# Performance work log

Measured on AMD Instinct MI355X. Metric: run time of the kernel, lower is better.

The kernel has to match this reference:

```python
import jax, jax.numpy as jnp
import numpy as np
from jax import lax


def setup_inputs() -> dict:
    key = jax.random.key(0)
    k1, k2, k3, k4 = jax.random.split(key, 4)
    H = 2048
    L = 3
    hidden_states = jax.random.normal(k1, (2, 4096, H), dtype=jnp.float32)
    Win = jax.random.normal(k2, (3 * H, H), dtype=jnp.float32) * (H ** -0.5)
    conv_w = jax.random.normal(k3, (H, 1, L), dtype=jnp.float32) * (L ** -0.5)
    Wout = jax.random.normal(k4, (H, H), dtype=jnp.float32) * (H ** -0.5)
    return {"hidden_states": hidden_states, "Win": Win, "conv_w": conv_w, "Wout": Wout}


def reference(hidden_states, Win, conv_w, Wout):
    H = hidden_states.shape[-1]
    L = conv_w.shape[-1]
    BCx = jnp.einsum('bsh,oh->bso', hidden_states, Win)  # (b, s, 3H)
    B, C, x = jnp.split(BCx, 3, axis=-1)
    Bx = jnp.transpose(B * x, (0, 2, 1))  # (b, H, s)
    # depthwise causal conv: left-pad L-1 so output length == s (torch pads both
    # sides then slices [..., :seqlen]; left-only padding is equivalent)
    conv_out = lax.conv_general_dilated(
        Bx, conv_w, window_strides=(1,), padding=[(L - 1, 0)],
        feature_group_count=H, dimension_numbers=('NCH', 'OIH', 'NCH'))
    y = C * jnp.transpose(conv_out, (0, 2, 1))  # (b, s, H)
    return jnp.einsum('bsh,oh->bso', y, Wout)
```

## Files before the change

kernel.cpp:

```cpp
#include <hip/hip_runtime.h>
#include <hip/hip_bf16.h>

typedef unsigned short u16;
typedef __attribute__((ext_vector_type(8))) short bf16x8;
typedef __attribute__((ext_vector_type(4))) float f32x4;

static __device__ __forceinline__ u16 f2bf(float f) {
    unsigned u = __float_as_uint(f);
    unsigned r = (u + 0x7fffu + ((u >> 16) & 1u)) >> 16;
    return (u16)r;
}
static __device__ __forceinline__ float bf2f(u16 u) {
    return __uint_as_float(((unsigned)u) << 16);
}

static __device__ __forceinline__ void async_copy16(const void* gptr, void* lptr) {
    __builtin_amdgcn_global_load_lds(
        (const __attribute__((address_space(1))) void*)gptr,
        (__attribute__((address_space(3))) void*)lptr, 16, 0, 0);
}

__global__ __launch_bounds__(256)
void cvt_all(const float* __restrict__ a, const float* __restrict__ b,
             const float* __restrict__ c,
             u16* __restrict__ oa, u16* __restrict__ ob, u16* __restrict__ oc) {
#pragma unroll
    for (int it = 0; it < 8; it++) {
        long li = ((long)it << 20) + (long)blockIdx.x * 256 + threadIdx.x;
        const float* src; u16* dst; long u;
        if (li < 4194304)      { src = a; dst = oa; u = li; }
        else if (li < 7340032) { src = b; dst = ob; u = li - 4194304; }
        else                   { src = c; dst = oc; u = li - 7340032; }
        long i = u * 4;
        float4 f = *(const float4*)(src + i);
        u16 o[4] = { f2bf(f.x), f2bf(f.y), f2bf(f.z), f2bf(f.w) };
        *(uint2*)(dst + i) = *(const uint2*)o;
    }
}

template<bool BF16_OUT>
__global__ __launch_bounds__(512, 2)
void gemm_bt8(const u16* __restrict__ A, const u16* __restrict__ B,
              void* __restrict__ Cout, int M, int N, int K) {
    __shared__ __align__(16) u16 lds[65536];

    const int t    = threadIdx.x;
    const int lane = t & 63;
    const int wm   = (t >> 6) >> 2;
    const int wn   = (t >> 6) & 3;
    const int l15  = lane & 15;
    const int hi   = lane >> 4;
    const int l7   = lane & 7;

    const int nCols = N >> 8;
    const int TPB   = nCols >> 3;
    const int xcd   = blockIdx.x & 7;
    const int slot  = blockIdx.x >> 3;
    const long rowA = (long)slot * 256;
    long rowB = (long)xcd * TPB * 256;

    const int pl0 = t >> 3;
    const int slotcol = ((t & 7) ^ (pl0 & 7)) * 8;
    const u16* Asrc[2][2];
    const u16* Bsrc[2][2];
#pragma unroll
    for (int h = 0; h < 2; h++) {
        Asrc[h][0] = A + (rowA + h * 64 + pl0) * (long)K + slotcol;
        Asrc[h][1] = A + (rowA + 128 + h * 64 + pl0) * (long)K + slotcol;
    }
    auto SET_B = [&](long rB) {
#pragma unroll
        for (int h = 0; h < 2; h++) {
            int nb = (pl0 >> 5) * 64 + h * 32 + (pl0 & 31);
            Bsrc[h][0] = B + (rB + nb) * (long)K + slotcol;
            Bsrc[h][1] = Bsrc[h][0] + 128 * (long)K;
        }
    };
    SET_B(rowB);
    const int t8 = t * 8;

    auto STAGE_A = [&](int bufo, int h, int kk) {
        u16* d = lds + bufo + h * 8192 + t8;
        async_copy16(Asrc[h][0] + kk, d);
        async_copy16(Asrc[h][1] + kk, d + 4096);
    };
    auto STAGE_B = [&](int bufo, int h, int kk) {
        u16* d = lds + bufo + 16384 + h * 8192 + t8;
        async_copy16(Bsrc[h][0] + kk, d);
        async_copy16(Bsrc[h][1] + kk, d + 4096);
    };

    const int aBase = wm * 4096 + l15 * 64;
    const int bBase = 16384 + wn * 2048 + l15 * 64;
    const int sOff0 = (hi ^ l7) * 8;
    const int sOff1 = ((4 + hi) ^ l7) * 8;

    bf16x8 af[4][2], ba[2][2], bb[2][2];
    f32x4 acc[8][4] = {};

    auto LOAD_A2 = [&](int bufo, int Mq, int mb) {
        const u16* p = lds + bufo + Mq * 8192 + aBase + mb * 1024;
        af[mb][0]     = *(const bf16x8*)(p + sOff0);
        af[mb][1]     = *(const bf16x8*)(p + sOff1);
        af[mb + 1][0] = *(const bf16x8*)(p + 1024 + sOff0);
        af[mb + 1][1] = *(const bf16x8*)(p + 1024 + sOff1);
    };
    auto LOAD_B = [&](bf16x8 (&bg)[2][2], int bufo, int Nq) {
        const u16* p = lds + bufo + Nq * 8192 + bBase;
        bg[0][0] = *(const bf16x8*)(p + sOff0);
        bg[0][1] = *(const bf16x8*)(p + sOff1);
        bg[1][0] = *(const bf16x8*)(p + 1024 + sOff0);
        bg[1][1] = *(const bf16x8*)(p + 1024 + sOff1);
    };
    auto MFMA_H = [&](int Mq, int Nq, int mb, bf16x8 (&bg)[2][2]) {
        __builtin_amdgcn_s_setprio(1);
#pragma unroll
        for (int ks = 0; ks < 2; ks++)
#pragma unroll
            for (int m = mb; m < mb + 2; m++)
#pragma unroll
                for (int n = 0; n < 2; n++)
                    acc[Mq * 4 + m][Nq * 2 + n] =
                        __builtin_amdgcn_mfma_f32_16x16x32_bf16(
                            af[m][ks], bg[n][ks], acc[Mq * 4 + m][Nq * 2 + n],
                            0, 0, 0);
        __builtin_amdgcn_s_setprio(0);
    };

#define BAR()   __builtin_amdgcn_s_barrier()
#define SB()    __builtin_amdgcn_sched_barrier(0)
#define LGKM(n) do { asm volatile("s_waitcnt lgkmcnt(" #n ")" ::: "memory"); \
                     __builtin_amdgcn_sched_barrier(0); } while (0)
#define VM(n)   asm volatile("s_waitcnt vmcnt(" #n ")" ::: "memory")

#define TILE(BC, BN, KK)                                                     \
                                                              \
    LOAD_B(ba, BC, 0); LOAD_A2(BC, 0, 0); SB(); LOAD_A2(BC, 0, 2);           \
    STAGE_A(BN, 0, KK); STAGE_B(BN, 0, KK);                                  \
    LGKM(4); MFMA_H(0, 0, 0, ba); LGKM(0); MFMA_H(0, 0, 2, ba); BAR();       \
                                                              \
    LOAD_B(bb, BC, 1);                                                       \
    STAGE_B(BN, 1, KK); STAGE_A(BN, 1, KK);                                  \
    LGKM(0); MFMA_H(0, 1, 0, bb); MFMA_H(0, 1, 2, bb); BAR();                \
                                                              \
    LOAD_A2(BC, 1, 0); SB(); LOAD_A2(BC, 1, 2);                              \
    LGKM(4); MFMA_H(1, 1, 0, bb); LGKM(0); MFMA_H(1, 1, 2, bb); BAR();       \
                                                              \
    VM(0);                                                                   \
    MFMA_H(1, 0, 0, ba); MFMA_H(1, 0, 2, ba); BAR();

    STAGE_A(0, 0, 0);  STAGE_B(0, 0, 0);
    STAGE_A(0, 1, 0);  STAGE_B(0, 1, 0);
    asm volatile("s_waitcnt vmcnt(0)" ::: "memory");
    BAR();

    const int NT = K >> 6;
#pragma unroll 1
    for (int j = 0; j < TPB; j++) {
        const long rowBc = rowB;
#pragma unroll 1
        for (int i = 0; i < NT - 2; i += 2) {
            TILE(0, 32768, (i + 1) << 6);
            TILE(32768, 0, (i + 2) << 6);
        }
        TILE(0, 32768, (NT - 1) << 6);
        if (j + 1 < TPB) { rowB += 256; SET_B(rowB); }
        TILE(32768, 0, 0);

        const long crowBase = rowA + wm * 128 + hi * 4;
        const long ccolBase = rowBc + wn * 64 + l15;
#pragma unroll
        for (int mi = 0; mi < 8; mi++) {
#pragma unroll
            for (int nj = 0; nj < 4; nj++) {
                long base = (crowBase + mi * 16) * N + ccolBase + nj * 16;
#pragma unroll
                for (int r = 0; r < 4; r++) {
                    float v = acc[mi][nj][r];
                    long idx = base + (long)r * N;
                    if (BF16_OUT) ((u16*)Cout)[idx] = f2bf(v);
                    else          ((float*)Cout)[idx] = v;
                }
            }
        }
        if (j + 1 < TPB) {
#pragma unroll
            for (int mi = 0; mi < 8; mi++)
#pragma unroll
                for (int nj = 0; nj < 4; nj++)
#pragma unroll
                    for (int r = 0; r < 4; r++)
                        acc[mi][nj][r] = 0.0f;
        }
    }
    asm volatile("s_waitcnt vmcnt(0) lgkmcnt(0)" ::: "memory");

#undef TILE
#undef VM
#undef LGKM
#undef SB
#undef BAR
}

union U16x8 { uint4 v; u16 u[8]; };

__global__ __launch_bounds__(256)
void conv_fuse(const u16* __restrict__ BCx, const float* __restrict__ cw,
               u16* __restrict__ y) {
    const int r0 = blockIdx.x * 4;
    const int h0 = threadIdx.x * 8;
    const int batch = r0 >> 12;

    U16x8 Bv[6], Xv[6], Cv[4];
#pragma unroll
    for (int ii = 0; ii < 6; ii++) {
        int g = r0 - 2 + ii;
        if (g >= 0 && (g >> 12) == batch) {
            const u16* rp = BCx + (long)g * 6144;
            Bv[ii].v = *(const uint4*)(rp + h0);
            Xv[ii].v = *(const uint4*)(rp + 4096 + h0);
        } else {
            Bv[ii].v = make_uint4(0, 0, 0, 0);
            Xv[ii].v = make_uint4(0, 0, 0, 0);
        }
    }
#pragma unroll
    for (int jj = 0; jj < 4; jj++)
        Cv[jj].v = *(const uint4*)(BCx + (long)(r0 + jj) * 6144 + 2048 + h0);

    float bx[6][8];
#pragma unroll
    for (int ii = 0; ii < 6; ii++)
#pragma unroll
        for (int i = 0; i < 8; i++)
            bx[ii][i] = bf2f(Bv[ii].u[i]) * bf2f(Xv[ii].u[i]);

    float w0[8], w1[8], w2[8];
#pragma unroll
    for (int i = 0; i < 8; i++) {
        int h = h0 + i;
        w0[i] = cw[h * 3];
        w1[i] = cw[h * 3 + 1];
        w2[i] = cw[h * 3 + 2];
    }

#pragma unroll
    for (int jj = 0; jj < 4; jj++) {
        U16x8 o;
#pragma unroll
        for (int i = 0; i < 8; i++) {
            float v = w2[i] * bx[jj + 2][i] + w1[i] * bx[jj + 1][i]
                    + w0[i] * bx[jj][i];
            o.u[i] = f2bf(v * bf2f(Cv[jj].u[i]));
        }
        *(uint4*)(y + (long)(r0 + jj) * 2048 + h0) = o.v;
    }
}

extern "C" void kernel_launch(void* const* d_in, const int* in_sizes, int n_in,
                              void* d_out, int out_size, void* d_ws, size_t ws_size,
                              hipStream_t stream) {
    const float* hs   = (const float*)d_in[0];
    const float* Win  = (const float*)d_in[1];
    const float* cw   = (const float*)d_in[2];
    const float* Wout = (const float*)d_in[3];
    float* out = (float*)d_out;

    char* ws = (char*)d_ws;
    u16* hsb   = (u16*)(ws);
    u16* Winb  = (u16*)(ws +  33554432);
    u16* Woutb = (u16*)(ws +  58720256);
    u16* bcx   = (u16*)(ws +  67108864);
    u16* yb    = (u16*)(ws + 167772160);

    cvt_all<<<4096, 256, 0, stream>>>(hs, Win, Wout, hsb, Winb, Woutb);

    gemm_bt8<true ><<<256, 512, 0, stream>>>(hsb, Winb, bcx, 8192, 6144, 2048);

    conv_fuse<<<2048, 256, 0, stream>>>(bcx, cw, yb);

    gemm_bt8<false><<<256, 512, 0, stream>>>(yb, Woutb, out, 8192, 2048, 2048);
}
```

Measured before the change: 445.2 us.

## Switch GEMM to one-tile-per-block grid with quarter-tile staged pipeline

Replaces the persistent loop, in which each block walked several N tiles, with a 2D grid where each block computes exactly one 256x256 output tile. Blocks are remapped so each XCD gets a contiguous range of columns. The K loop is restructured so smaller quarter-tiles are staged, with vmcnt(6) waits instead of full drains and more barriers per step. The aim is to keep more global loads in flight and overlap them better with MFMA, at the cost of more barriers and losing the reuse of the A tile across N tiles.

```diff
diff --git a/kernel.cpp b/kernel.cpp
--- a/kernel.cpp
+++ b/kernel.cpp
@@ -52,31 +52,24 @@
     const int hi   = lane >> 4;
     const int l7   = lane & 7;
 
-    const int nCols = N >> 8;
-    const int TPB   = nCols >> 3;
-    const int xcd   = blockIdx.x & 7;
-    const int slot  = blockIdx.x >> 3;
-    const long rowA = (long)slot * 256;
-    long rowB = (long)xcd * TPB * 256;
+    const int id   = blockIdx.y * gridDim.x + blockIdx.x;
+    const int cpx  = gridDim.x >> 3;
+    const int bx   = (id & 7) * cpx + ((id >> 3) % cpx);
+    const int by   = (id >> 3) / cpx;
+    const long rowA = (long)by * 256;
+    const long rowB = (long)bx * 256;
 
     const int pl0 = t >> 3;
     const int slotcol = ((t & 7) ^ (pl0 & 7)) * 8;
-    const u16* Asrc[2][2];
-    const u16* Bsrc[2][2];
+    const u16* Asrc[2][2]; const u16* Bsrc[2][2];
 #pragma unroll
     for (int h = 0; h < 2; h++) {
         Asrc[h][0] = A + (rowA + h * 64 + pl0) * (long)K + slotcol;
         Asrc[h][1] = A + (rowA + 128 + h * 64 + pl0) * (long)K + slotcol;
-    }
-    auto SET_B = [&](long rB) {
-#pragma unroll
-        for (int h = 0; h < 2; h++) {
-            int nb = (pl0 >> 5) * 64 + h * 32 + (pl0 & 31);
-            Bsrc[h][0] = B + (rB + nb) * (long)K + slotcol;
-            Bsrc[h][1] = Bsrc[h][0] + 128 * (long)K;
-        }
-    };
-    SET_B(rowB);
+        int nB0 = (pl0 >> 5) * 64 + h * 32 + (pl0 & 31);
+        Bsrc[h][0] = B + (rowB + nB0) * (long)K + slotcol;
+        Bsrc[h][1] = Bsrc[h][0] + 128 * (long)K;
+    }
     const int t8 = t * 8;
 
     auto STAGE_A = [&](int bufo, int h, int kk) {
@@ -98,12 +91,13 @@
     bf16x8 af[4][2], ba[2][2], bb[2][2];
     f32x4 acc[8][4] = {};
 
-    auto LOAD_A2 = [&](int bufo, int Mq, int mb) {
-        const u16* p = lds + bufo + Mq * 8192 + aBase + mb * 1024;
-        af[mb][0]     = *(const bf16x8*)(p + sOff0);
-        af[mb][1]     = *(const bf16x8*)(p + sOff1);
-        af[mb + 1][0] = *(const bf16x8*)(p + 1024 + sOff0);
-        af[mb + 1][1] = *(const bf16x8*)(p + 1024 + sOff1);
+    auto LOAD_A4 = [&](int bufo, int Mq) {
+        const u16* p = lds + bufo + Mq * 8192 + aBase;
+#pragma unroll
+        for (int m = 0; m < 4; m++) {
+            af[m][0] = *(const bf16x8*)(p + m * 1024 + sOff0);
+            af[m][1] = *(const bf16x8*)(p + m * 1024 + sOff1);
+        }
     };
     auto LOAD_B = [&](bf16x8 (&bg)[2][2], int bufo, int Nq) {
         const u16* p = lds + bufo + Nq * 8192 + bBase;
@@ -112,12 +106,12 @@
         bg[1][0] = *(const bf16x8*)(p + 1024 + sOff0);
         bg[1][1] = *(const bf16x8*)(p + 1024 + sOff1);
     };
-    auto MFMA_H = [&](int Mq, int Nq, int mb, bf16x8 (&bg)[2][2]) {
+    auto MFMA_Q = [&](int Mq, int Nq, bf16x8 (&bg)[2][2]) {
         __builtin_amdgcn_s_setprio(1);
 #pragma unroll
         for (int ks = 0; ks < 2; ks++)
 #pragma unroll
-            for (int m = mb; m < mb + 2; m++)
+            for (int m = 0; m < 4; m++)
 #pragma unroll
                 for (int n = 0; n < 2; n++)
                     acc[Mq * 4 + m][Nq * 2 + n] =
@@ -128,78 +122,68 @@
     };
 
 #define BAR()   __builtin_amdgcn_s_barrier()
-#define SB()    __builtin_amdgcn_sched_barrier(0)
-#define LGKM(n) do { asm volatile("s_waitcnt lgkmcnt(" #n ")" ::: "memory"); \
+#define LGKMZ() do { asm volatile("s_waitcnt lgkmcnt(0)" ::: "memory");      \
                      __builtin_amdgcn_sched_barrier(0); } while (0)
-#define VM(n)   asm volatile("s_waitcnt vmcnt(" #n ")" ::: "memory")
-
-#define TILE(BC, BN, KK)                                                     \
-                                                              \
-    LOAD_B(ba, BC, 0); LOAD_A2(BC, 0, 0); SB(); LOAD_A2(BC, 0, 2);           \
-    STAGE_A(BN, 0, KK); STAGE_B(BN, 0, KK);                                  \
-    LGKM(4); MFMA_H(0, 0, 0, ba); LGKM(0); MFMA_H(0, 0, 2, ba); BAR();       \
-                                                              \
-    LOAD_B(bb, BC, 1);                                                       \
-    STAGE_B(BN, 1, KK); STAGE_A(BN, 1, KK);                                  \
-    LGKM(0); MFMA_H(0, 1, 0, bb); MFMA_H(0, 1, 2, bb); BAR();                \
-                                                              \
-    LOAD_A2(BC, 1, 0); SB(); LOAD_A2(BC, 1, 2);                              \
-    LGKM(4); MFMA_H(1, 1, 0, bb); LGKM(0); MFMA_H(1, 1, 2, bb); BAR();       \
-                                                              \
-    VM(0);                                                                   \
-    MFMA_H(1, 0, 0, ba); MFMA_H(1, 0, 2, ba); BAR();
-
-    STAGE_A(0, 0, 0);  STAGE_B(0, 0, 0);
-    STAGE_A(0, 1, 0);  STAGE_B(0, 1, 0);
-    asm volatile("s_waitcnt vmcnt(0)" ::: "memory");
+#define VM6()   asm volatile("s_waitcnt vmcnt(6)" ::: "memory")
+
+    STAGE_A(0, 0, 0);      STAGE_A(0, 1, 0);
+    STAGE_B(0, 0, 0);      STAGE_B(0, 1, 0);
+    STAGE_A(32768, 0, 64); STAGE_B(32768, 0, 64); STAGE_B(32768, 1, 64);
+    VM6();
     BAR();
 
     const int NT = K >> 6;
+    const int NI = NT >> 1;
 #pragma unroll 1
-    for (int j = 0; j < TPB; j++) {
-        const long rowBc = rowB;
-#pragma unroll 1
-        for (int i = 0; i < NT - 2; i += 2) {
-            TILE(0, 32768, (i + 1) << 6);
-            TILE(32768, 0, (i + 2) << 6);
-        }
-        TILE(0, 32768, (NT - 1) << 6);
-        if (j + 1 < TPB) { rowB += 256; SET_B(rowB); }
-        TILE(32768, 0, 0);
-
-        const long crowBase = rowA + wm * 128 + hi * 4;
-        const long ccolBase = rowBc + wn * 64 + l15;
-#pragma unroll
-        for (int mi = 0; mi < 8; mi++) {
-#pragma unroll
-            for (int nj = 0; nj < 4; nj++) {
-                long base = (crowBase + mi * 16) * N + ccolBase + nj * 16;
-#pragma unroll
-                for (int r = 0; r < 4; r++) {
-                    float v = acc[mi][nj][r];
-                    long idx = base + (long)r * N;
-                    if (BF16_OUT) ((u16*)Cout)[idx] = f2bf(v);
-                    else          ((float*)Cout)[idx] = v;
-                }
+    for (int i = 0; i < NI; i++) {
+        const int kk1 = ((i << 1) + 1) << 6;
+        int kk2 = ((i << 1) + 2) << 6; if (kk2 >= K) kk2 = 0;
+        int kk3 = ((i << 1) + 3) << 6; if (kk3 >= K) kk3 = 0;
+        LOAD_A4(0, 0); LOAD_B(ba, 0, 0);
+        STAGE_A(32768, 1, kk1);
+        BAR(); LGKMZ(); MFMA_Q(0, 0, ba); BAR();
+        LOAD_B(bb, 0, 1);
+        STAGE_A(0, 0, kk2);
+        BAR(); LGKMZ(); MFMA_Q(0, 1, bb); BAR();
+        LOAD_A4(0, 1);
+        STAGE_B(0, 0, kk2);
+        BAR(); LGKMZ(); MFMA_Q(1, 1, bb); BAR();
+        STAGE_B(0, 1, kk2);
+        BAR(); LGKMZ(); MFMA_Q(1, 0, ba); VM6(); BAR();
+        LOAD_A4(32768, 0); LOAD_B(ba, 32768, 0);
+        STAGE_A(0, 1, kk2);
+        BAR(); LGKMZ(); MFMA_Q(0, 0, ba); BAR();
+        LOAD_B(bb, 32768, 1);
+        STAGE_A(32768, 0, kk3);
+        BAR(); LGKMZ(); MFMA_Q(0, 1, bb); BAR();
+        LOAD_A4(32768, 1);
+        STAGE_B(32768, 0, kk3);
+        BAR(); LGKMZ(); MFMA_Q(1, 1, bb); BAR();
+        STAGE_B(32768, 1, kk3);
+        BAR(); LGKMZ(); MFMA_Q(1, 0, ba); VM6(); BAR();
+    }
+    asm volatile("s_waitcnt vmcnt(0) lgkmcnt(0)" ::: "memory");
+
+#undef BAR
+#undef LGKMZ
+#undef VM6
+
+    const long crowBase = rowA + wm * 128 + hi * 4;
+    const long ccolBase = rowB + wn * 64 + l15;
+#pragma unroll
+    for (int mi = 0; mi < 8; mi++) {
+#pragma unroll
+        for (int nj = 0; nj < 4; nj++) {
+            long base = (crowBase + mi * 16) * N + ccolBase + nj * 16;
+#pragma unroll
+            for (int r = 0; r < 4; r++) {
+                float v = acc[mi][nj][r];
+                long idx = base + (long)r * N;
+                if (BF16_OUT) ((u16*)Cout)[idx] = f2bf(v);
+                else          ((float*)Cout)[idx] = v;
             }
         }
-        if (j + 1 < TPB) {
-#pragma unroll
-            for (int mi = 0; mi < 8; mi++)
-#pragma unroll
-                for (int nj = 0; nj < 4; nj++)
-#pragma unroll
-                    for (int r = 0; r < 4; r++)
-                        acc[mi][nj][r] = 0.0f;
-        }
-    }
-    asm volatile("s_waitcnt vmcnt(0) lgkmcnt(0)" ::: "memory");
-
-#undef TILE
-#undef VM
-#undef LGKM
-#undef SB
-#undef BAR
+    }
 }
 
 union U16x8 { uint4 v; u16 u[8]; };
@@ -275,9 +259,9 @@
 
     cvt_all<<<4096, 256, 0, stream>>>(hs, Win, Wout, hsb, Winb, Woutb);
 
-    gemm_bt8<true ><<<256, 512, 0, stream>>>(hsb, Winb, bcx, 8192, 6144, 2048);
+    gemm_bt8<true ><<<dim3(24, 32), 512, 0, stream>>>(hsb, Winb, bcx, 8192, 6144, 2048);
 
     conv_fuse<<<2048, 256, 0, stream>>>(bcx, cw, yb);
 
-    gemm_bt8<false><<<256, 512, 0, stream>>>(yb, Woutb, out, 8192, 2048, 2048);
-}
+    gemm_bt8<false><<<dim3(8, 32), 512, 0, stream>>>(yb, Woutb, out, 8192, 2048, 2048);
+}
```

Measured after the change: 427.8 us. 1.04x faster.

## Launch one GEMM block per output tile with XCD-aware mapping and finer staging

Applied to the files above, without the earlier changes.

The persistent per-block loop over several B column tiles is replaced by a 2D grid that gives each block exactly one 256x256 output tile. Block ids are remapped so tiles sharing B columns land on the same XCD. The async LDS staging is spread across the four phases of each k-tile with partial vmcnt waits instead of one full drain. Epilogue stores become nontemporal. For the first GEMM this raises the block count from 256 to 768, which improves load balance and latency hiding but drops the persistent reuse of the A tile across column tiles.

```diff
diff --git a/kernel.cpp b/kernel.cpp
--- a/kernel.cpp
+++ b/kernel.cpp
@@ -52,31 +52,26 @@
     const int hi   = lane >> 4;
     const int l7   = lane & 7;
 
-    const int nCols = N >> 8;
-    const int TPB   = nCols >> 3;
-    const int xcd   = blockIdx.x & 7;
-    const int slot  = blockIdx.x >> 3;
-    const long rowA = (long)slot * 256;
-    long rowB = (long)xcd * TPB * 256;
+    const int id   = blockIdx.y * gridDim.x + blockIdx.x;
+    const int cpx  = gridDim.x >> 3;
+    const int bx   = (id & 7) * cpx + ((id >> 3) % cpx);
+    const int by   = (id >> 3) / cpx;
+    const long rowA = (long)by * 256;
+    const long rowB = (long)bx * 256;
 
     const int pl0 = t >> 3;
     const int slotcol = ((t & 7) ^ (pl0 & 7)) * 8;
-    const u16* Asrc[2][2];
-    const u16* Bsrc[2][2];
+    const u16* Asrc[2][2]; const u16* Bsrc[2][2];
 #pragma unroll
     for (int h = 0; h < 2; h++) {
-        Asrc[h][0] = A + (rowA + h * 64 + pl0) * (long)K + slotcol;
-        Asrc[h][1] = A + (rowA + 128 + h * 64 + pl0) * (long)K + slotcol;
-    }
-    auto SET_B = [&](long rB) {
-#pragma unroll
-        for (int h = 0; h < 2; h++) {
-            int nb = (pl0 >> 5) * 64 + h * 32 + (pl0 & 31);
-            Bsrc[h][0] = B + (rB + nb) * (long)K + slotcol;
-            Bsrc[h][1] = Bsrc[h][0] + 128 * (long)K;
-        }
-    };
-    SET_B(rowB);
+        int gA0 = h * 64 + pl0;
+        int gA1 = 128 + h * 64 + pl0;
+        Asrc[h][0] = A + (rowA + gA0) * (long)K + slotcol;
+        Asrc[h][1] = A + (rowA + gA1) * (long)K + slotcol;
+        int nB0 = (pl0 >> 5) * 64 + h * 32 + (pl0 & 31);
+        Bsrc[h][0] = B + (rowB + nB0) * (long)K + slotcol;
+        Bsrc[h][1] = B + (rowB + nB0 + 128) * (long)K + slotcol;
+    }
     const int t8 = t * 8;
 
     auto STAGE_A = [&](int bufo, int h, int kk) {
@@ -136,17 +131,18 @@
 #define TILE(BC, BN, KK)                                                     \
                                                               \
     LOAD_B(ba, BC, 0); LOAD_A2(BC, 0, 0); SB(); LOAD_A2(BC, 0, 2);           \
-    STAGE_A(BN, 0, KK); STAGE_B(BN, 0, KK);                                  \
+    STAGE_A(BN, 0, KK); VM(2);                                               \
     LGKM(4); MFMA_H(0, 0, 0, ba); LGKM(0); MFMA_H(0, 0, 2, ba); BAR();       \
                                                               \
     LOAD_B(bb, BC, 1);                                                       \
-    STAGE_B(BN, 1, KK); STAGE_A(BN, 1, KK);                                  \
+    STAGE_B(BN, 0, KK);                                                      \
     LGKM(0); MFMA_H(0, 1, 0, bb); MFMA_H(0, 1, 2, bb); BAR();                \
                                                               \
     LOAD_A2(BC, 1, 0); SB(); LOAD_A2(BC, 1, 2);                              \
+    STAGE_A(BN, 1, KK);                                                      \
     LGKM(4); MFMA_H(1, 1, 0, bb); LGKM(0); MFMA_H(1, 1, 2, bb); BAR();       \
                                                               \
-    VM(0);                                                                   \
+    STAGE_B(BN, 1, KK); VM(4);                                               \
     MFMA_H(1, 0, 0, ba); MFMA_H(1, 0, 2, ba); BAR();
 
     STAGE_A(0, 0, 0);  STAGE_B(0, 0, 0);
@@ -156,42 +152,11 @@
 
     const int NT = K >> 6;
 #pragma unroll 1
-    for (int j = 0; j < TPB; j++) {
-        const long rowBc = rowB;
-#pragma unroll 1
-        for (int i = 0; i < NT - 2; i += 2) {
-            TILE(0, 32768, (i + 1) << 6);
-            TILE(32768, 0, (i + 2) << 6);
-        }
-        TILE(0, 32768, (NT - 1) << 6);
-        if (j + 1 < TPB) { rowB += 256; SET_B(rowB); }
-        TILE(32768, 0, 0);
-
-        const long crowBase = rowA + wm * 128 + hi * 4;
-        const long ccolBase = rowBc + wn * 64 + l15;
-#pragma unroll
-        for (int mi = 0; mi < 8; mi++) {
-#pragma unroll
-            for (int nj = 0; nj < 4; nj++) {
-                long base = (crowBase + mi * 16) * N + ccolBase + nj * 16;
-#pragma unroll
-                for (int r = 0; r < 4; r++) {
-                    float v = acc[mi][nj][r];
-                    long idx = base + (long)r * N;
-                    if (BF16_OUT) ((u16*)Cout)[idx] = f2bf(v);
-                    else          ((float*)Cout)[idx] = v;
-                }
-            }
-        }
-        if (j + 1 < TPB) {
-#pragma unroll
-            for (int mi = 0; mi < 8; mi++)
-#pragma unroll
-                for (int nj = 0; nj < 4; nj++)
-#pragma unroll
-                    for (int r = 0; r < 4; r++)
-                        acc[mi][nj][r] = 0.0f;
-        }
+    for (int i = 0; i < NT; i += 2) {
+        int k1 = (i + 1) << 6;
+        int k2 = (i + 2 < NT) ? (i + 2) << 6 : 0;
+        TILE(0, 32768, k1);
+        TILE(32768, 0, k2);
     }
     asm volatile("s_waitcnt vmcnt(0) lgkmcnt(0)" ::: "memory");
 
@@ -200,6 +165,25 @@
 #undef LGKM
 #undef SB
 #undef BAR
+
+    const long crowBase = rowA + wm * 128 + hi * 4;
+    const long ccolBase = rowB + wn * 64 + l15;
+#pragma unroll
+    for (int mi = 0; mi < 8; mi++) {
+#pragma unroll
+        for (int nj = 0; nj < 4; nj++) {
+            long base = (crowBase + mi * 16) * N + ccolBase + nj * 16;
+#pragma unroll
+            for (int r = 0; r < 4; r++) {
+                float v = acc[mi][nj][r];
+                long idx = base + (long)r * N;
+                if (BF16_OUT)
+                    __builtin_nontemporal_store(f2bf(v), (u16*)Cout + idx);
+                else
+                    __builtin_nontemporal_store(v, (float*)Cout + idx);
+            }
+        }
+    }
 }
 
 union U16x8 { uint4 v; u16 u[8]; };
@@ -275,9 +259,9 @@
 
     cvt_all<<<4096, 256, 0, stream>>>(hs, Win, Wout, hsb, Winb, Woutb);
 
-    gemm_bt8<true ><<<256, 512, 0, stream>>>(hsb, Winb, bcx, 8192, 6144, 2048);
+    gemm_bt8<true ><<<dim3(24, 32), 512, 0, stream>>>(hsb, Winb, bcx, 8192, 6144, 2048);
 
     conv_fuse<<<2048, 256, 0, stream>>>(bcx, cw, yb);
 
-    gemm_bt8<false><<<256, 512, 0, stream>>>(yb, Woutb, out, 8192, 2048, 2048);
-}
+    gemm_bt8<false><<<dim3(8, 32), 512, 0, stream>>>(yb, Woutb, out, 8192, 2048, 2048);
+}
```

Result: slower. 499.8 us (+12.3%).
